# Kernel optimization log

Hardware: AMD Instinct MI355X
Metric: run time of the kernel (lower is better)

## Reference

```python
import jax, jax.numpy as jnp
import numpy as np

N = 100000
E = 1600000
IN_DIM = 128
HID_DIM = 128
NUM_CLASSES = 40


def setup_inputs() -> dict:
    key = jax.random.key(0)
    k1, k2, k3, k4, k5, k6 = jax.random.split(key, 6)
    x = jax.random.normal(k1, (N, IN_DIM), dtype=jnp.float32)
    e = jax.random.randint(k2, (2, E), 0, N, dtype=jnp.int64)
    s1 = 1.0 / np.sqrt(IN_DIM)
    s2 = 1.0 / np.sqrt(HID_DIM)
    W1 = jax.random.uniform(k3, (IN_DIM, HID_DIM), jnp.float32, -s1, s1)
    b1 = jax.random.uniform(k4, (HID_DIM,), jnp.float32, -s1, s1)
    W2 = jax.random.uniform(k5, (HID_DIM, NUM_CLASSES), jnp.float32, -s2, s2)
    b2 = jax.random.uniform(k6, (NUM_CLASSES,), jnp.float32, -s2, s2)
    return {"x": x, "e": e, "W1": W1, "b1": b1, "W2": W2, "b2": b2}


def _gcn_conv(x, src, dst, norm, W, b, n):
    # linear transform first (PyG GCNConv), then normalized aggregation
    h = x @ W                                    # [N, d_out]
    out = jax.ops.segment_sum(h[src] * norm[:, None], dst, num_segments=n)
    return out + b


def reference(x, e, W1, b1, W2, b2):
    n = x.shape[0]
    loop = jnp.arange(n, dtype=e.dtype)
    src = jnp.concatenate([e[0], loop])          # add self-loops
    dst = jnp.concatenate([e[1], loop])
    deg = jax.ops.segment_sum(jnp.ones_like(dst, dtype=x.dtype), dst, num_segments=n)
    d_inv_sqrt = deg ** -0.5                     # deg >= 1 due to self-loops
    norm = d_inv_sqrt[src] * d_inv_sqrt[dst]     # symmetric normalization
    h = jax.nn.relu(_gcn_conv(x, src, dst, norm, W1, b1, n))
    return _gcn_conv(h, src, dst, norm, W2, b2, n)
```

## Files before the change

kernel.cpp:

```cpp
#include <hip/hip_runtime.h>


typedef unsigned int u32;
typedef unsigned short u16;
typedef __attribute__((ext_vector_type(8))) short short8;
typedef __attribute__((ext_vector_type(4))) float floatx4;

#define CHUNK 4096

#define REP7(M)  M(0) M(1) M(2) M(3) M(4) M(5) M(6)
#define REP8(M)  M(0) M(1) M(2) M(3) M(4) M(5) M(6) M(7)
#define REP15(M) REP8(M) M(8) M(9) M(10) M(11) M(12) M(13) M(14)
#define REP16(M) REP15(M) M(15)

static __device__ inline u16 f2bf(float f) {
    u32 u = __float_as_uint(f);
    return (u16)((u + 0x7FFFu + ((u >> 16) & 1u)) >> 16);
}
static __device__ inline u32 pack2(float a, float b) {
    return (u32)f2bf(a) | ((u32)f2bf(b) << 16);
}
static __device__ inline float bflo(u32 u) { return __uint_as_float(u << 16); }
static __device__ inline float bfhi(u32 u) { return __uint_as_float(u & 0xffff0000u); }

static __device__ inline bool detect_is64(const int* e32, int lane) {
    bool nz = e32[2 * lane + 1] != 0;
    return __ballot(nz) == 0ull;
}

__global__ void k_prepW(const float* __restrict__ W1, const float* __restrict__ W2,
                        u16* __restrict__ WTb, u16* __restrict__ W2Tb) {
    int id = blockIdx.x * 256 + threadIdx.x;
    if (id < 16384) {
        int k = id >> 7, c = id & 127;
        WTb[c * 128 + k] = f2bf(W1[id]);
    } else {
        int id2 = id - 16384;
        if (id2 < 6144) {
            int c = id2 >> 7, k = id2 & 127;
            W2Tb[id2] = f2bf(c < 40 ? W2[k * 40 + c] : 0.f);
        }
    }
}

__global__ __launch_bounds__(256) void k_front(const void* __restrict__ e_raw,
                                               int E, int NC, int NB,
                                               int* __restrict__ histG,
                                               const float* __restrict__ X,
                                               const u16* __restrict__ WTb,
                                               u16* __restrict__ H1s, int n) {
    __shared__ u32 smem[64 * 68 + 128 * 68];
    const int tid = threadIdx.x;
    if ((int)blockIdx.x < NC) {
        int* h = (int*)smem;
        h[tid] = 0; h[tid + 256] = 0;
        __syncthreads();
        const int* e32 = (const int*)e_raw;
        bool is64 = detect_is64(e32, tid & 63);
        int c = blockIdx.x;
        int j0 = c * CHUNK, j1 = min(E, j0 + CHUNK);
        for (int j = j0 + tid; j < j1; j += 256) {
            int d = is64 ? (int)((const long long*)e_raw)[E + j] : e32[E + j];
            atomicAdd(&h[d >> 8], 1);
        }
        __syncthreads();
        for (int b = tid; b < NB; b += 256) histG[(size_t)b * NC + c] = h[b];
        return;
    }
    u32* As = smem;
    u32* Bs = smem + 64 * 68;
    const int row0 = ((int)blockIdx.x - NC) * 64;
#pragma unroll
    for (int it = 0; it < 8; it++) {
        int i = tid + it * 256;
        int r = i >> 5;
        int c4 = (i & 31) << 2;
        int gr = row0 + r;
        float4 v = make_float4(0.f, 0.f, 0.f, 0.f);
        if (gr < n) v = *(const float4*)(X + (size_t)gr * 128 + c4);
        uint2 p;
        p.x = pack2(v.x, v.y);
        p.y = pack2(v.z, v.w);
        *(uint2*)&As[r * 68 + (c4 >> 1)] = p;
    }
#pragma unroll
    for (int it = 0; it < 8; it++) {
        int i = tid + it * 256;
        int r = i >> 4;
        int c4 = (i & 15) << 2;
        *(uint4*)&Bs[r * 68 + c4] =
            *(const uint4*)((const u32*)WTb + (size_t)r * 64 + c4);
    }
    __syncthreads();

    const int lane = tid & 63;
    const int wave = tid >> 6;
    const int wr = wave >> 1;
    const int wc = wave & 1;
    const int mrow = lane & 15;
    const int quad = lane >> 4;

    floatx4 acc[2][4] = {};
    for (int k0 = 0; k0 < 128; k0 += 32) {
        int koff = (k0 >> 1) + quad * 4;
        short8 a[2], b[4];
#pragma unroll
        for (int i = 0; i < 2; i++)
            a[i] = *(const short8*)&As[((wr * 2 + i) * 16 + mrow) * 68 + koff];
#pragma unroll
        for (int j = 0; j < 4; j++)
            b[j] = *(const short8*)&Bs[((wc * 4 + j) * 16 + mrow) * 68 + koff];
#pragma unroll
        for (int i = 0; i < 2; i++)
#pragma unroll
            for (int j = 0; j < 4; j++)
                acc[i][j] = __builtin_amdgcn_mfma_f32_16x16x32_bf16(
                    a[i], b[j], acc[i][j], 0, 0, 0);
    }
#pragma unroll
    for (int i = 0; i < 2; i++) {
        int gr0 = row0 + (wr * 2 + i) * 16 + quad * 4;
#pragma unroll
        for (int j = 0; j < 4; j++) {
            u16* dst = H1s + (size_t)(wc * 4 + j) * ((size_t)n * 16);
#pragma unroll
            for (int rg = 0; rg < 4; rg++) {
                int grow = gr0 + rg;
                if (grow < n)
                    dst[(size_t)grow * 16 + mrow] = f2bf(acc[i][j][rg]);
            }
        }
    }
}

__global__ void k_scan1(const int* __restrict__ in, int* __restrict__ out,
                        int* __restrict__ bsum, int n) {
    __shared__ int sh[256];
    int i = blockIdx.x * 256 + threadIdx.x;
    int v = (i < n) ? in[i] : 0;
    sh[threadIdx.x] = v;
    __syncthreads();
    for (int off = 1; off < 256; off <<= 1) {
        int t = (threadIdx.x >= off) ? sh[threadIdx.x - off] : 0;
        __syncthreads();
        sh[threadIdx.x] += t;
        __syncthreads();
    }
    if (i < n) out[i] = sh[threadIdx.x] - v;
    if (threadIdx.x == 255) bsum[blockIdx.x] = sh[255];
}

__global__ void k_scan2(int* __restrict__ bsum, int nb) {
    __shared__ int sh[1024];
    int t = threadIdx.x;
    int v = (t < nb) ? bsum[t] : 0;
    sh[t] = v;
    __syncthreads();
    for (int off = 1; off < 1024; off <<= 1) {
        int u = (t >= off) ? sh[t - off] : 0;
        __syncthreads();
        sh[t] += u;
        __syncthreads();
    }
    if (t < nb) bsum[t] = sh[t] - v;
}

__global__ __launch_bounds__(256) void k_place(const void* __restrict__ e_raw,
                                               const int* __restrict__ histOff,
                                               const int* __restrict__ bsumH,
                                               u32* __restrict__ tmp,
                                               int E, int NB, int NC) {
    __shared__ int cur[512];
    int c = blockIdx.x;
    int t = threadIdx.x;
    for (int b = t; b < NB; b += 256) {
        int idx = b * NC + c;
        cur[b] = histOff[idx] + bsumH[idx >> 8];
    }
    __syncthreads();
    const int* e32 = (const int*)e_raw;
    bool is64 = detect_is64(e32, t & 63);
    int j0 = c * CHUNK, j1 = min(E, j0 + CHUNK);
    for (int j = j0 + t; j < j1; j += 256) {
        int s, d;
        if (is64) {
            s = (int)((const long long*)e_raw)[j];
            d = (int)((const long long*)e_raw)[E + j];
        } else {
            s = e32[j];
            d = e32[E + j];
        }
        int pos = atomicAdd(&cur[d >> 8], 1);
        tmp[pos] = (u32)s | ((u32)(d & 255) << 24);
    }
}

__global__ __launch_bounds__(256) void k_degsort(const u32* __restrict__ tmp,
                                                 const int* __restrict__ histOff,
                                                 const int* __restrict__ bsumH,
                                                 int* __restrict__ degI,
                                                 float* __restrict__ dinv,
                                                 int* __restrict__ rs,
                                                 int* __restrict__ eSrc,
                                                 int n, int NB, int NC, int E) {
    __shared__ int cnt[256];
    __shared__ int sh[256];
    __shared__ int cur[256];
    int b = blockIdx.x;
    int t = threadIdx.x;
    cnt[t] = 0;
    __syncthreads();
    int i0 = b * NC;
    int seg0 = histOff[i0] + bsumH[i0 >> 8];
    int seg1 = E;
    if (b + 1 < NB) {
        int i1 = (b + 1) * NC;
        seg1 = histOff[i1] + bsumH[i1 >> 8];
    }
    for (int j = seg0 + t; j < seg1; j += 256) atomicAdd(&cnt[tmp[j] >> 24], 1);
    __syncthreads();
    int v = cnt[t];
    sh[t] = v;
    __syncthreads();
    for (int off = 1; off < 256; off <<= 1) {
        int u = (t >= off) ? sh[t - off] : 0;
        __syncthreads();
        sh[t] += u;
        __syncthreads();
    }
    int myStart = seg0 + sh[t] - v;
    cur[t] = myStart;
    int node = b * 256 + t;
    if (node < n) {
        degI[node] = v;
        dinv[node] = rsqrtf((float)v + 1.0f);
        rs[node] = myStart;
    }
    __syncthreads();
    for (int j = seg0 + t; j < seg1; j += 256) {
        u32 rec = tmp[j];
        int dl = rec >> 24;
        int s = (int)(rec & 0x00FFFFFFu);
        int pos = atomicAdd(&cur[dl], 1);
        eSrc[pos] = s;
    }
}

__global__ __launch_bounds__(256) void k_ew(int* __restrict__ eSrc,
                                            const float* __restrict__ dinv,
                                            int E) {
    int i = blockIdx.x * 256 + threadIdx.x;
    if (i >= E) return;
    u32 s = (u32)eSrc[i];
    u32 wq = (u32)__float2int_rn(dinv[s] * 32767.f);
    eSrc[i] = (int)(s | (wq << 17));
}

__global__ __launch_bounds__(256) void k_gather128(
    const u32* __restrict__ Hb, const int* __restrict__ rs,
    const int* __restrict__ degI, const u32* __restrict__ eW,
    const float* __restrict__ b1, u32* __restrict__ outb, int n) {
    const int lane = threadIdx.x & 63;
    const int wave = threadIdx.x >> 6;
    const int g = lane >> 3;
    const int l = lane & 7;
    const int slice = blockIdx.x & 7;
    const int chunk = blockIdx.x >> 3;
    const u32* __restrict__ Hu = Hb + (size_t)slice * ((size_t)n * 8);

    const int node = chunk * 32 + wave * 8 + g;
    if (node >= n) return;
    const int start = rs[node];
    const int deg = degI[node];
    float ax = 0.f, ay = 0.f;
    u32 r0, r1, r2, r3, r4, r5, r6, r7, r8, r9, r10, r11, r12, r13, r14, r15;
    u32 u0, u1, u2, u3, u4, u5, u6, u7, u8, u9, u10, u11, u12, u13, u14, u15;
    float w0, w1, w2, w3, w4, w5, w6, w7, w8, w9, w10, w11, w12, w13, w14, w15;
    int t = 0;

#define GW(K)  w##K = (float)(r##K >> 17);
#define GH(K)  u##K = Hu[((r##K & 0x1FFFFu) << 3) + l];
#define GF(K)  r##K = eW[bq + K];
#define GA(K)  ax = fmaf(w##K, bflo(u##K), ax); ay = fmaf(w##K, bfhi(u##K), ay);

    if (deg >= 16) {
        int bq = start;
        REP16(GF)
        for (; t + 32 <= deg; t += 16) {
            REP16(GW)
            REP16(GH)
            bq = start + t + 16;
            REP16(GF)
            REP16(GA)
        }
        REP16(GW)
        REP16(GH)
        REP16(GA)
        t += 16;
    }
    if (t < deg) {
        const int bq = start + t;
        const int rm = deg - t - 1;
#define GTF(K) r##K = eW[bq + min(K, rm)];
#define GTW(K) w##K = (K <= rm) ? (float)(r##K >> 17) : 0.f;
        REP15(GTF)
        REP15(GTW)
        REP15(GH)
        REP15(GA)
#undef GTF
#undef GTW
    }
#undef GW
#undef GH
#undef GF
#undef GA
    ax *= (1.f / 32767.f);
    ay *= (1.f / 32767.f);
    const float di = rsqrtf((float)deg + 1.0f);
    const u32 us = Hu[(node << 3) + l];
    const float2 bv = *(const float2*)(b1 + (slice * 8 + l) * 2);
    float inx = fmaf(di, bflo(us), ax);
    float iny = fmaf(di, bfhi(us), ay);
    float rx = fmaxf(fmaf(di, inx, bv.x), 0.f);
    float ry = fmaxf(fmaf(di, iny, bv.y), 0.f);
    outb[(size_t)node * 64 + slice * 8 + l] = pack2(rx, ry);
}

__global__ __launch_bounds__(256) void k_gemm2(const u32* __restrict__ A1b,
                                               const u16* __restrict__ W2Tb,
                                               const float* __restrict__ dinv,
                                               u16* __restrict__ H2s, int n) {
    __shared__ u32 As[64 * 68];
    __shared__ u32 Bs[48 * 68];
    const int tid = threadIdx.x;
    const int row0 = blockIdx.x * 64;
#pragma unroll
    for (int it = 0; it < 4; it++) {
        int i = tid + it * 256;
        int r = i >> 4;
        int c4 = (i & 15) << 2;
        int gr = row0 + r;
        uint4 v = make_uint4(0u, 0u, 0u, 0u);
        if (gr < n) v = *(const uint4*)(A1b + (size_t)gr * 64 + c4);
        *(uint4*)&As[r * 68 + c4] = v;
    }
#pragma unroll
    for (int it = 0; it < 3; it++) {
        int i = tid + it * 256;
        int r = i >> 4;
        int c4 = (i & 15) << 2;
        *(uint4*)&Bs[r * 68 + c4] =
            *(const uint4*)((const u32*)W2Tb + (size_t)r * 64 + c4);
    }
    __syncthreads();

    const int lane = tid & 63;
    const int wave = tid >> 6;
    const int mrow = lane & 15;
    const int quad = lane >> 4;

    floatx4 acc[3] = {};
    for (int k0 = 0; k0 < 128; k0 += 32) {
        int koff = (k0 >> 1) + quad * 4;
        short8 a = *(const short8*)&As[(wave * 16 + mrow) * 68 + koff];
#pragma unroll
        for (int j = 0; j < 3; j++) {
            short8 b = *(const short8*)&Bs[(j * 16 + mrow) * 68 + koff];
            acc[j] = __builtin_amdgcn_mfma_f32_16x16x32_bf16(a, b, acc[j], 0, 0, 0);
        }
    }
    int gr0 = row0 + wave * 16 + quad * 4;
    float dv[4];
#pragma unroll
    for (int rg = 0; rg < 4; rg++)
        dv[rg] = (gr0 + rg < n) ? dinv[gr0 + rg] : 0.f;
#pragma unroll
    for (int j = 0; j < 3; j++) {
        int gcol = j * 16 + mrow;
        if (gcol < 40) {
#pragma unroll
            for (int rg = 0; rg < 4; rg++) {
                int grow = gr0 + rg;
                if (grow < n)
                    H2s[(size_t)grow * 40 + gcol] = f2bf(dv[rg] * acc[j][rg]);
            }
        }
    }
}

__global__ __launch_bounds__(256) void k_gather40(
    const u32* __restrict__ H2b, const int* __restrict__ rs,
    const int* __restrict__ degI, const u32* __restrict__ eW,
    const float* __restrict__ dinv, const float* __restrict__ b2,
    float* __restrict__ out, int n) {
    const int wave = threadIdx.x >> 6;
    const int lane = threadIdx.x & 63;
    const int node = blockIdx.x * 4 + wave;
    if (node >= n) return;
    if (lane >= 60) return;
    const int g = lane / 20;
    const int l = lane - g * 20;
    const int start = rs[node];
    const int deg = degI[node];
    const int c0 = (deg * g) / 3;
    const int c1 = (deg * (g + 1)) / 3;
    const int cnt = c1 - c0;
    const int sb = start + c0;
    float ax = 0.f, ay = 0.f;
    u32 r0, r1, r2, r3, r4, r5, r6, r7;
    u32 u0, u1, u2, u3, u4, u5, u6, u7;
    int t = 0;

#define QH(K) u##K = H2b[(r##K & 0x1FFFFu) * 20 + l];
#define QF(K) r##K = eW[bq + K];
#define QA(K) ax += bflo(u##K); ay += bfhi(u##K);

    if (cnt >= 8) {
        int bq = sb;
        REP8(QF)
        for (; t + 16 <= cnt; t += 8) {
            REP8(QH)
            bq = sb + t + 8;
            REP8(QF)
            REP8(QA)
        }
        REP8(QH)
        REP8(QA)
        t += 8;
    }
    if (t < cnt) {
        const int bq = sb + t;
        const int rm = cnt - t - 1;
#define QTF(K) r##K = eW[bq + min(K, rm)];
#define QTM(K) if (K > rm) u##K = 0u;
        REP7(QTF)
        REP7(QH)
        REP7(QTM)
        REP7(QA)
#undef QTF
#undef QTM
    }
#undef QH
#undef QF
#undef QA
    float x1 = __shfl(ax, (lane + 20) & 63), y1 = __shfl(ay, (lane + 20) & 63);
    float x2 = __shfl(ax, (lane + 40) & 63), y2 = __shfl(ay, (lane + 40) & 63);
    if (lane < 20) {
        float di = dinv[node];
        u32 u = H2b[(size_t)node * 20 + l];
        float2 bv = *(const float2*)(b2 + l * 2);
        float ox = fmaf(di, ax + x1 + x2 + bflo(u), bv.x);
        float oy = fmaf(di, ay + y1 + y2 + bfhi(u), bv.y);
        *(float2*)(out + (size_t)node * 40 + l * 2) = make_float2(ox, oy);
    }
}

extern "C" void kernel_launch(void* const* d_in, const int* in_sizes, int n_in,
                              void* d_out, int out_size, void* d_ws, size_t ws_size,
                              hipStream_t stream) {
    const float* x  = (const float*)d_in[0];
    const void*  e  = d_in[1];
    const float* W1 = (const float*)d_in[2];
    const float* b1 = (const float*)d_in[3];
    const float* W2 = (const float*)d_in[4];
    const float* b2 = (const float*)d_in[5];
    float* out = (float*)d_out;

    const int n = in_sizes[0] / 128;
    const int E = in_sizes[1] / 2;
    const int NB = (n + 255) / 256;
    const int NC = (E + CHUNK - 1) / CHUNK;
    const int NH = NB * NC;
    const int nbH = (NH + 255) / 256;
    const int G1 = (n + 63) / 64;

    int*   degI    = (int*)d_ws;
    int*   rs      = degI + n;
    int*   bsumH   = rs + n;
    float* dinv    = (float*)(bsumH + 1024);
    int*   histG   = (int*)(dinv + n);
    int*   histOff = histG + NH;
    size_t off = (size_t)((char*)(histOff + NH) - (char*)d_ws);
    off = (off + 15) & ~(size_t)15;
    u16*   WTb    = (u16*)((char*)d_ws + off);
    u16*   W2Tb   = WTb + 16384;
    off = (size_t)((char*)(W2Tb + 6144) - (char*)d_ws);
    off = (off + 15) & ~(size_t)15;
    u32*   tmp    = (u32*)((char*)d_ws + off);
    int*   eSrc   = (int*)(tmp + (size_t)E);
    u16*   H1s    = (u16*)(eSrc + (size_t)E);
    u32*   H1b    = (u32*)H1s;
    u32*   A1b    = (u32*)(H1s + (size_t)n * 128);
    u16*   H2s    = (u16*)(A1b + (size_t)n * 64);
    u32*   H2b    = (u32*)H2s;

    k_prepW<<<88, 256, 0, stream>>>(W1, W2, WTb, W2Tb);
    k_front<<<NC + G1, 256, 0, stream>>>(e, E, NC, NB, histG, x, WTb, H1s, n);

    k_scan1<<<nbH, 256, 0, stream>>>(histG, histOff, bsumH, NH);
    k_scan2<<<1, 1024, 0, stream>>>(bsumH, nbH);
    k_place<<<NC, 256, 0, stream>>>(e, histOff, bsumH, tmp, E, NB, NC);

    k_degsort<<<NB, 256, 0, stream>>>(tmp, histOff, bsumH, degI, dinv, rs,
                                      eSrc, n, NB, NC, E);
    k_ew<<<(E + 255) / 256, 256, 0, stream>>>(eSrc, dinv, E);

    k_gather128<<<8 * ((n + 31) / 32), 256, 0, stream>>>(H1b, rs, degI,
                                                         (const u32*)eSrc,
                                                         b1, A1b, n);
    k_gemm2<<<(n + 63) / 64, 256, 0, stream>>>(A1b, W2Tb, dinv, H2s, n);
    k_gather40<<<(n + 3) / 4, 256, 0, stream>>>(H2b, rs, degI, (const u32*)eSrc,
                                                dinv, b2, out, n);
}
```

Measured before the change: 317.7 us.

## Stage neighbor gathers through LDS with async global_load_lds double buffering

Rewrites the layer-1 gather kernel so that neighbor feature rows are fetched with global_load_lds directly into a per-wave double-buffered LDS stage. Edge records are loaded cooperatively, eight per group, and broadcast with shuffles, with manual vmcnt waits to overlap the next batch's loads with the current accumulation. All groups in a wave now iterate to the wave's maximum degree in batches of eight, replacing the per-thread 16-deep register unrolling. This aims to cut register pressure and keep more loads in flight, at the cost of masked work for low-degree nodes and fragile hand-written wait counts.

```diff
diff --git a/kernel.cpp b/kernel.cpp
--- a/kernel.cpp
+++ b/kernel.cpp
@@ -5,13 +5,13 @@
 typedef unsigned short u16;
 typedef __attribute__((ext_vector_type(8))) short short8;
 typedef __attribute__((ext_vector_type(4))) float floatx4;
+typedef __attribute__((address_space(3))) u32 as3u;
+typedef __attribute__((address_space(1))) const u32 as1u;
 
 #define CHUNK 4096
 
 #define REP7(M)  M(0) M(1) M(2) M(3) M(4) M(5) M(6)
 #define REP8(M)  M(0) M(1) M(2) M(3) M(4) M(5) M(6) M(7)
-#define REP15(M) REP8(M) M(8) M(9) M(10) M(11) M(12) M(13) M(14)
-#define REP16(M) REP15(M) M(15)
 
 static __device__ inline u16 f2bf(float f) {
     u32 u = __float_as_uint(f);
@@ -260,64 +260,85 @@
     const u32* __restrict__ Hb, const int* __restrict__ rs,
     const int* __restrict__ degI, const u32* __restrict__ eW,
     const float* __restrict__ b1, u32* __restrict__ outb, int n) {
+    __shared__ u32 stage[4][2][8][64];
     const int lane = threadIdx.x & 63;
     const int wave = threadIdx.x >> 6;
     const int g = lane >> 3;
     const int l = lane & 7;
+    const int gbase = lane & 56;
     const int slice = blockIdx.x & 7;
     const int chunk = blockIdx.x >> 3;
-    const u32* __restrict__ Hu = Hb + (size_t)slice * ((size_t)n * 8);
+    const u32* __restrict__ Hs = Hb + (size_t)slice * ((size_t)n * 8);
 
     const int node = chunk * 32 + wave * 8 + g;
+    int start = 0, deg = 0;
+    if (node < n) { start = rs[node]; deg = degI[node]; }
+    int dmax = deg;
+#pragma unroll
+    for (int off = 8; off < 64; off <<= 1)
+        dmax = max(dmax, __shfl_xor(dmax, off));
+    const int nb = (dmax + 7) >> 3;
+
+    float ax = 0.f, ay = 0.f;
+    if (nb > 0) {
+        const int dm = (deg > 0) ? deg - 1 : 0;
+        auto LDR = [&](int t) -> u32 { return eW[start + min(t + l, dm)]; };
+        auto WX = [&](u32 r, int t) -> float {
+            return (t + l < deg) ? (float)(r >> 17) : 0.f;
+        };
+        auto ISSUE = [&](u32 rv, int bf) {
+#pragma unroll
+            for (int k = 0; k < 8; k++) {
+                int sk = __shfl((int)rv, gbase + k);
+                const u32* gp = Hs + (((size_t)(sk & 0x1FFFF)) << 3) + l;
+                __builtin_amdgcn_global_load_lds(
+                    (as1u*)gp, (as3u*)&stage[wave][bf][k][0], 4, 0, 0);
+            }
+        };
+        u32 rA = LDR(0);
+        asm volatile("s_waitcnt vmcnt(0)" ::: "memory");
+        float wA = WX(rA, 0);
+        float wB = 0.f;
+        u32 rB = LDR(8);
+        __builtin_amdgcn_sched_barrier(0);
+        ISSUE(rA, 0);
+        for (int i = 0; i < nb; i++) {
+            const int bsel = i & 1;
+            const int t1 = (i + 1) << 3, t2 = (i + 2) << 3;
+            asm volatile("s_waitcnt vmcnt(8)" ::: "memory");
+            __builtin_amdgcn_sched_barrier(0);
+            if (bsel == 0) {
+                wB = WX(rB, t1);
+                u32 rv = rB;
+                rA = LDR(t2);
+                __builtin_amdgcn_sched_barrier(0);
+                ISSUE(rv, 1);
+            } else {
+                wA = WX(rA, t1);
+                u32 rv = rA;
+                rB = LDR(t2);
+                __builtin_amdgcn_sched_barrier(0);
+                ISSUE(rv, 0);
+            }
+            asm volatile("s_waitcnt vmcnt(9)" ::: "memory");
+            __builtin_amdgcn_sched_barrier(0);
+            const float wf = bsel ? wB : wA;
+#pragma unroll
+            for (int k = 0; k < 8; k++) {
+                u32 u = stage[wave][bsel][k][lane];
+                float wk = __shfl(wf, gbase + k);
+                ax = fmaf(wk, bflo(u), ax);
+                ay = fmaf(wk, bfhi(u), ay);
+            }
+        }
+        asm volatile("s_waitcnt vmcnt(0)" ::: "memory");
+        __builtin_amdgcn_sched_barrier(0);
+    }
     if (node >= n) return;
-    const int start = rs[node];
-    const int deg = degI[node];
-    float ax = 0.f, ay = 0.f;
-    u32 r0, r1, r2, r3, r4, r5, r6, r7, r8, r9, r10, r11, r12, r13, r14, r15;
-    u32 u0, u1, u2, u3, u4, u5, u6, u7, u8, u9, u10, u11, u12, u13, u14, u15;
-    float w0, w1, w2, w3, w4, w5, w6, w7, w8, w9, w10, w11, w12, w13, w14, w15;
-    int t = 0;
-
-#define GW(K)  w##K = (float)(r##K >> 17);
-#define GH(K)  u##K = Hu[((r##K & 0x1FFFFu) << 3) + l];
-#define GF(K)  r##K = eW[bq + K];
-#define GA(K)  ax = fmaf(w##K, bflo(u##K), ax); ay = fmaf(w##K, bfhi(u##K), ay);
-
-    if (deg >= 16) {
-        int bq = start;
-        REP16(GF)
-        for (; t + 32 <= deg; t += 16) {
-            REP16(GW)
-            REP16(GH)
-            bq = start + t + 16;
-            REP16(GF)
-            REP16(GA)
-        }
-        REP16(GW)
-        REP16(GH)
-        REP16(GA)
-        t += 16;
-    }
-    if (t < deg) {
-        const int bq = start + t;
-        const int rm = deg - t - 1;
-#define GTF(K) r##K = eW[bq + min(K, rm)];
-#define GTW(K) w##K = (K <= rm) ? (float)(r##K >> 17) : 0.f;
-        REP15(GTF)
-        REP15(GTW)
-        REP15(GH)
-        REP15(GA)
-#undef GTF
-#undef GTW
-    }
-#undef GW
-#undef GH
-#undef GF
-#undef GA
     ax *= (1.f / 32767.f);
     ay *= (1.f / 32767.f);
     const float di = rsqrtf((float)deg + 1.0f);
-    const u32 us = Hu[(node << 3) + l];
+    const u32 us = Hs[((size_t)node << 3) + l];
     const float2 bv = *(const float2*)(b1 + (slice * 8 + l) * 2);
     float inx = fmaf(di, bflo(us), ax);
     float iny = fmaf(di, bfhi(us), ay);
```

New measurement: 338.8 us. 1.07x slower.
